# Kernel tuning notes

Hardware: AMD Instinct MI355X
Metric: run time of the kernel (lower is better)

## Reference

```python
import jax, jax.numpy as jnp
import numpy as np

N = 50000
E = 600000
D_IN = 128
D_HID = 128


def gcn_conv(x, src, dst, ew, W, b):
    """PyG-style GCNConv with self-loops and symmetric normalization.
    x: [N, Fin], src/dst: [E'], ew: [E'], W: [Fin, Fout], b: [Fout].
    """
    n = x.shape[0]
    # degree from incoming edge weights (self-loops already appended)
    deg = jax.ops.segment_sum(ew, dst, num_segments=n)
    dinv = jnp.where(deg > 0, jax.lax.rsqrt(deg), 0.0)
    norm = dinv[src] * ew * dinv[dst]  # [E']
    h = x @ W  # linear transform first (PyG order)
    msg = h[src] * norm[:, None]  # gather + scale, [E', Fout]
    out = jax.ops.segment_sum(msg, dst, num_segments=n)  # scatter-add
    return out + b


def setup_inputs() -> dict:
    key = jax.random.key(0)
    k1, k2, k3, k4, k5, k6, k7 = jax.random.split(key, 7)
    x = jax.random.normal(k1, (N, D_IN), dtype=jnp.float32)
    edge_index = jax.random.randint(k2, (2, E), 0, N, dtype=jnp.int64)
    edge_weight = jax.random.uniform(k3, (E,), dtype=jnp.float32)
    s1 = 1.0 / np.sqrt(D_IN)
    s2 = 1.0 / np.sqrt(D_HID)
    W1 = jax.random.uniform(k4, (D_IN, D_HID), dtype=jnp.float32, minval=-s1, maxval=s1)
    b1 = jax.random.uniform(k5, (D_HID,), dtype=jnp.float32, minval=-s1, maxval=s1)
    W2 = jax.random.uniform(k6, (D_HID, D_IN), dtype=jnp.float32, minval=-s2, maxval=s2)
    b2 = jax.random.uniform(k7, (D_IN,), dtype=jnp.float32, minval=-s2, maxval=s2)
    return {"x": x, "edge_index": edge_index, "edge_weight": edge_weight,
            "W1": W1, "b1": b1, "W2": W2, "b2": b2}


def reference(x, edge_index, edge_weight, W1, b1, W2, b2):
    n = x.shape[0]
    loops = jnp.arange(n, dtype=edge_index.dtype)
    src = jnp.concatenate([edge_index[0], loops])
    dst = jnp.concatenate([edge_index[1], loops])
    ew = jnp.concatenate([edge_weight, jnp.ones((n,), dtype=edge_weight.dtype)])
    h = gcn_conv(x, src, dst, ew, W1, b1)
    h = jax.nn.relu(h)
    h = gcn_conv(h, src, dst, ew, W2, b2)
    return jax.nn.sigmoid(h)
```

## Files before the change

kernel.cpp:

```cpp
#include <hip/hip_runtime.h>
#include <math.h>


typedef unsigned int uint32;
typedef unsigned long long u64;
typedef __attribute__((ext_vector_type(8))) short bf16x8;
typedef __attribute__((ext_vector_type(4))) float f32x4;
typedef __attribute__((ext_vector_type(2))) float f32x2;

__device__ __forceinline__ unsigned short f2bf(float f) {
    uint32 b = __float_as_uint(f);
    return (unsigned short)((b + 0x7FFFu + ((b >> 16) & 1u)) >> 16);
}

__device__ __forceinline__ float2 bf2_decode(uint32 u) {
    return make_float2(__uint_as_float(u << 16),
                       __uint_as_float(u & 0xFFFF0000u));
}

template <int AFP32, int OUTFP8>
__device__ __forceinline__ void gemm_body(const void* __restrict__ Ap,
                                          const unsigned short* __restrict__ WT,
                                          void* __restrict__ H,
                                          int n, int tb) {
    const int lane = threadIdx.x & 63;
    const int wv   = threadIdx.x >> 6;
    const int quad = lane >> 4;
    const int l16  = lane & 15;
    const int m0   = tb * 128 + wv * 32;
    f32x4 acc[2][8] = {};

    #pragma unroll
    for (int ks = 0; ks < 4; ++ks) {
        const int k0 = ks * 32 + quad * 8;
        bf16x8 a[2];
        #pragma unroll
        for (int rt = 0; rt < 2; ++rt) {
            int row = m0 + rt * 16 + l16;
            if (row >= n) row = n - 1;
            if (AFP32) {
                const float* Af = (const float*)Ap + (size_t)row * 128 + k0;
                float4 f0 = *(const float4*)(Af);
                float4 f1 = *(const float4*)(Af + 4);
                bf16x8 v;
                v[0] = (short)f2bf(f0.x); v[1] = (short)f2bf(f0.y);
                v[2] = (short)f2bf(f0.z); v[3] = (short)f2bf(f0.w);
                v[4] = (short)f2bf(f1.x); v[5] = (short)f2bf(f1.y);
                v[6] = (short)f2bf(f1.z); v[7] = (short)f2bf(f1.w);
                a[rt] = v;
            } else {
                const unsigned short* Ab = (const unsigned short*)Ap + (size_t)row * 128 + k0;
                a[rt] = *(const bf16x8*)Ab;
            }
        }
        #pragma unroll
        for (int ct = 0; ct < 8; ++ct) {
            bf16x8 b = *(const bf16x8*)(WT + (size_t)(ct * 16 + l16) * 128 + k0);
            acc[0][ct] = __builtin_amdgcn_mfma_f32_16x16x32_bf16(a[0], b, acc[0][ct], 0, 0, 0);
            acc[1][ct] = __builtin_amdgcn_mfma_f32_16x16x32_bf16(a[1], b, acc[1][ct], 0, 0, 0);
        }
    }

    #pragma unroll
    for (int rt = 0; rt < 2; ++rt) {
        #pragma unroll
        for (int r = 0; r < 4; ++r) {
            int row = m0 + rt * 16 + quad * 4 + r;
            if (row < n) {
                if (OUTFP8) {
                    unsigned char* o = (unsigned char*)H + (size_t)row * 128 + l16;
                    #pragma unroll
                    for (int cp = 0; cp < 4; ++cp) {
                        int pk = __builtin_amdgcn_cvt_pk_fp8_f32(
                            acc[rt][2 * cp][r], acc[rt][2 * cp + 1][r], 0, false);
                        o[(2 * cp) * 16]     = (unsigned char)(pk & 0xFF);
                        o[(2 * cp + 1) * 16] = (unsigned char)((pk >> 8) & 0xFF);
                    }
                } else {
                    unsigned short* o = (unsigned short*)H + (size_t)row * 128 + l16;
                    #pragma unroll
                    for (int ct = 0; ct < 8; ++ct)
                        o[ct * 16] = f2bf(acc[rt][ct][r]);
                }
            }
        }
    }
}

__global__ __launch_bounds__(256) void k_init(u64* __restrict__ packed, int n4,
                                              int* __restrict__ done,
                                              const float* __restrict__ W1,
                                              const float* __restrict__ W2,
                                              unsigned short* __restrict__ WT1,
                                              unsigned short* __restrict__ WT2) {
    int idx = blockIdx.x * 256 + threadIdx.x;
    if (idx < n4) ((uint4*)packed)[idx] = make_uint4(0u, 0u, 0u, 0u);
    if (idx == 0) *done = 0;
    if (blockIdx.x < 64) {
        int j = blockIdx.x * 256 + threadIdx.x;
        int k = j >> 7, nn = j & 127;
        WT1[nn * 128 + k] = f2bf(W1[k * 128 + nn]);
        WT2[nn * 128 + k] = f2bf(W2[k * 128 + nn]);
    }
}

__global__ __launch_bounds__(256) void k_gemm1_hist(const float* __restrict__ x,
                                                    const unsigned short* __restrict__ WT1,
                                                    unsigned char* __restrict__ h8,
                                                    const int* __restrict__ dst,
                                                    const float* __restrict__ ew,
                                                    u64* __restrict__ packed,
                                                    int* __restrict__ rank,
                                                    int E, int N, int gGemm) {
    const int b = blockIdx.x;
    if (b < gGemm) {
        gemm_body<1, 1>(x, WT1, h8, N, b);
        return;
    }
    int i = (b - gGemm) * 256 + threadIdx.x;
    if (i < E) {
        int d = dst[i];
        int r = (i >> 8) & 7;
        u64 add = (1ULL << 44) + (u64)(ew[i] * 4294967296.0f);
        u64 old = atomicAdd(&packed[(size_t)r * N + d], add);
        rank[i] = (int)(old >> 44);
    }
}

__global__ __launch_bounds__(256) void k_scan(const u64* __restrict__ packed,
                                              float* __restrict__ dinv,
                                              u64* __restrict__ bases,
                                              int* __restrict__ rowptr,
                                              int* __restrict__ csums,
                                              int* __restrict__ done, int nNodes) {
    __shared__ int s[256];
    __shared__ int lastFlag;
    const int t = threadIdx.x;
    const int base = blockIdx.x * 1024 + t * 4;
    const int n = nNodes + 1;
    int v[4];
    #pragma unroll
    for (int u = 0; u < 4; ++u) {
        int idx = base + u;
        int c = 0;
        if (idx < nNodes) {
            const u64 mask = (1ULL << 44) - 1;
            u64 ssum = 0;
            u64 bs = 0;
            uint32 cum = 0;
            #pragma unroll
            for (int r = 0; r < 8; ++r) {
                u64 pv = packed[(size_t)r * nNodes + idx];
                bs |= (u64)cum << (8 * r);
                cum += (uint32)(pv >> 44);
                ssum += (pv & mask);
            }
            c = (int)cum;
            float deg = 1.0f + (float)ssum * (1.0f / 4294967296.0f);
            dinv[idx] = rsqrtf(deg);
            bases[idx] = bs;
        }
        v[u] = c;
    }
    s[t] = v[0] + v[1] + v[2] + v[3];
    __syncthreads();
    #pragma unroll
    for (int off = 1; off < 256; off <<= 1) {
        int x = (t >= off) ? s[t - off] : 0;
        __syncthreads();
        s[t] += x;
        __syncthreads();
    }
    if (t == 255)
        __hip_atomic_store(&csums[blockIdx.x], s[255], __ATOMIC_RELEASE,
                           __HIP_MEMORY_SCOPE_AGENT);
    int e = (t == 0) ? 0 : s[t - 1];
    if (base + 0 < n) rowptr[base + 0] = e;
    if (base + 1 < n) rowptr[base + 1] = e + v[0];
    if (base + 2 < n) rowptr[base + 2] = e + v[0] + v[1];
    if (base + 3 < n) rowptr[base + 3] = e + v[0] + v[1] + v[2];

    __syncthreads();
    if (t == 0) {
        int prev = __hip_atomic_fetch_add(done, 1, __ATOMIC_ACQ_REL,
                                          __HIP_MEMORY_SCOPE_AGENT);
        lastFlag = (prev == (int)gridDim.x - 1);
    }
    __syncthreads();
    if (lastFlag && t < 64) {
        int g = (int)gridDim.x;
        int orig = (t < g) ? __hip_atomic_load(&csums[t], __ATOMIC_ACQUIRE,
                                               __HIP_MEMORY_SCOPE_AGENT)
                           : 0;
        int vv = orig;
        #pragma unroll
        for (int off = 1; off < 64; off <<= 1) {
            int y = __shfl_up(vv, off, 64);
            if (t >= off) vv += y;
        }
        if (t < g) csums[t] = vv - orig;
    }
}

__global__ __launch_bounds__(256) void k_fill(const int* __restrict__ src,
                                              const int* __restrict__ dst,
                                              const float* __restrict__ ew,
                                              const float* __restrict__ dinv,
                                              const int* __restrict__ rowptr,
                                              const int* __restrict__ csums,
                                              const u64* __restrict__ bases,
                                              const int* __restrict__ rank,
                                              float2* __restrict__ csr, int e) {
    int i = blockIdx.x * 256 + threadIdx.x;
    if (i < e) {
        int s = src[i], d = dst[i];
        int r = (i >> 8) & 7;
        float nrm = dinv[s] * ew[i] * dinv[d];
        int pos = rowptr[d] + csums[d >> 10]
                + (int)((bases[d] >> (8 * r)) & 0xFF) + rank[i];
        csr[pos] = make_float2(__int_as_float(s), nrm);
    }
}

__device__ __forceinline__ void fma8_bf(float* acc, uint4 u, float w) {
    float2 f;
    f = bf2_decode(u.x); acc[0] += f.x * w; acc[1] += f.y * w;
    f = bf2_decode(u.y); acc[2] += f.x * w; acc[3] += f.y * w;
    f = bf2_decode(u.z); acc[4] += f.x * w; acc[5] += f.y * w;
    f = bf2_decode(u.w); acc[6] += f.x * w; acc[7] += f.y * w;
}

__device__ __forceinline__ void fma8_f8(float* acc, uint2 u, float w) {
    f32x2 f;
    f = __builtin_amdgcn_cvt_pk_f32_fp8((int)u.x, false);
    acc[0] += f[0] * w; acc[1] += f[1] * w;
    f = __builtin_amdgcn_cvt_pk_f32_fp8((int)u.x, true);
    acc[2] += f[0] * w; acc[3] += f[1] * w;
    f = __builtin_amdgcn_cvt_pk_f32_fp8((int)u.y, false);
    acc[4] += f[0] * w; acc[5] += f[1] * w;
    f = __builtin_amdgcn_cvt_pk_f32_fp8((int)u.y, true);
    acc[6] += f[0] * w; acc[7] += f[1] * w;
}

__global__ __launch_bounds__(256) void k_ag2(const unsigned char* __restrict__ h8,
                                             const float2* __restrict__ csr,
                                             const int* __restrict__ rowptr,
                                             const int* __restrict__ csums,
                                             const float* __restrict__ dinv,
                                             const float4* __restrict__ bias4,
                                             const unsigned short* __restrict__ WT2,
                                             unsigned short* __restrict__ h2,
                                             int N) {
    __shared__ unsigned short sA[16][136];
    const int lane = threadIdx.x & 63;
    const int wv   = threadIdx.x >> 6;
    const int q    = lane >> 4;
    const int l    = lane & 15;
    const int nb   = blockIdx.x * 16;
    const uint2* H2 = (const uint2*)h8;

    for (int j = 0; j < 4; ++j) {
        const int node = nb + wv * 4 + j;
        float acc[8] = {};
        if (node < N) {
            const int start = rowptr[node] + csums[node >> 10];
            const int end   = rowptr[node + 1] + csums[(node + 1) >> 10];
            float di = dinv[node];
            float selfw = (q == 0) ? di * di : 0.0f;
            fma8_f8(acc, H2[(size_t)node * 16 + l], selfw);

            for (int k = start; k < end; k += 16) {
                float2 c[4];
                float w[4];
                #pragma unroll
                for (int jj = 0; jj < 4; ++jj) {
                    int ej = k + q + 4 * jj;
                    c[jj] = csr[ej < end ? ej : end - 1];
                    w[jj] = (ej < end) ? c[jj].y : 0.0f;
                }
                uint2 u[4];
                #pragma unroll
                for (int jj = 0; jj < 4; ++jj)
                    u[jj] = H2[(size_t)__float_as_int(c[jj].x) * 16 + l];
                #pragma unroll
                for (int jj = 0; jj < 4; ++jj) fma8_f8(acc, u[jj], w[jj]);
            }
            #pragma unroll
            for (int t = 0; t < 8; ++t) {
                acc[t] += __shfl_xor(acc[t], 16, 64);
                acc[t] += __shfl_xor(acc[t], 32, 64);
            }
        }
        if (q == 0) {
            uint4 o = make_uint4(0u, 0u, 0u, 0u);
            if (node < N) {
                float4 b0 = bias4[l * 2], b1v = bias4[l * 2 + 1];
                acc[0] += b0.x;  acc[1] += b0.y;  acc[2] += b0.z;  acc[3] += b0.w;
                acc[4] += b1v.x; acc[5] += b1v.y; acc[6] += b1v.z; acc[7] += b1v.w;
                #pragma unroll
                for (int t = 0; t < 8; ++t) acc[t] = fmaxf(acc[t], 0.0f);
                o.x = (uint32)f2bf(acc[0]) | ((uint32)f2bf(acc[1]) << 16);
                o.y = (uint32)f2bf(acc[2]) | ((uint32)f2bf(acc[3]) << 16);
                o.z = (uint32)f2bf(acc[4]) | ((uint32)f2bf(acc[5]) << 16);
                o.w = (uint32)f2bf(acc[6]) | ((uint32)f2bf(acc[7]) << 16);
            }
            *(uint4*)&sA[wv * 4 + j][l * 8] = o;
        }
    }

    __syncthreads();

    f32x4 a2[2] = {};
    #pragma unroll
    for (int ks = 0; ks < 4; ++ks) {
        const int k0 = ks * 32 + q * 8;
        bf16x8 a = *(const bf16x8*)&sA[l][k0];
        #pragma unroll
        for (int ct = 0; ct < 2; ++ct) {
            bf16x8 b = *(const bf16x8*)(WT2 + (size_t)(wv * 32 + ct * 16 + l) * 128 + k0);
            a2[ct] = __builtin_amdgcn_mfma_f32_16x16x32_bf16(a, b, a2[ct], 0, 0, 0);
        }
    }
    #pragma unroll
    for (int r = 0; r < 4; ++r) {
        int row = nb + q * 4 + r;
        if (row < N) {
            unsigned short* o = h2 + (size_t)row * 128 + wv * 32 + l;
            o[0]  = f2bf(a2[0][r]);
            o[16] = f2bf(a2[1][r]);
        }
    }
}

template <int INFP8, int ACT>
__global__ __launch_bounds__(256) void k_gather(const void* __restrict__ Hp,
                                                const float2* __restrict__ csr,
                                                const int* __restrict__ rowptr,
                                                const int* __restrict__ csums,
                                                const float* __restrict__ dinv,
                                                const float4* __restrict__ bias4,
                                                void* __restrict__ outp, int N) {
    int node = blockIdx.x * 4 + (threadIdx.x >> 6);
    if (node >= N) return;
    const int lane = threadIdx.x & 63;
    const int q = lane >> 4, l = lane & 15;
    const int start = rowptr[node] + csums[node >> 10];
    const int end   = rowptr[node + 1] + csums[(node + 1) >> 10];

    const uint2* H2 = (const uint2*)Hp;
    const uint4* H4 = (const uint4*)Hp;

    float di = dinv[node];
    float selfw = (q == 0) ? di * di : 0.0f;
    float acc[8] = {};
    if (INFP8) fma8_f8(acc, H2[(size_t)node * 16 + l], selfw);
    else       fma8_bf(acc, H4[(size_t)node * 16 + l], selfw);

    for (int k = start; k < end; k += 16) {
        float2 c[4];
        float w[4];
        #pragma unroll
        for (int j = 0; j < 4; ++j) {
            int ej = k + q + 4 * j;
            c[j] = csr[ej < end ? ej : end - 1];
            w[j] = (ej < end) ? c[j].y : 0.0f;
        }
        if (INFP8) {
            uint2 u[4];
            #pragma unroll
            for (int j = 0; j < 4; ++j)
                u[j] = H2[(size_t)__float_as_int(c[j].x) * 16 + l];
            #pragma unroll
            for (int j = 0; j < 4; ++j) fma8_f8(acc, u[j], w[j]);
        } else {
            uint4 u[4];
            #pragma unroll
            for (int j = 0; j < 4; ++j)
                u[j] = H4[(size_t)__float_as_int(c[j].x) * 16 + l];
            #pragma unroll
            for (int j = 0; j < 4; ++j) fma8_bf(acc, u[j], w[j]);
        }
    }

    #pragma unroll
    for (int j = 0; j < 8; ++j) {
        acc[j] += __shfl_xor(acc[j], 16, 64);
        acc[j] += __shfl_xor(acc[j], 32, 64);
    }

    if (q == 0) {
        float4 b0 = bias4[l * 2], b1 = bias4[l * 2 + 1];
        acc[0] += b0.x; acc[1] += b0.y; acc[2] += b0.z; acc[3] += b0.w;
        acc[4] += b1.x; acc[5] += b1.y; acc[6] += b1.z; acc[7] += b1.w;
        if (ACT == 0) {
            #pragma unroll
            for (int j = 0; j < 8; ++j) acc[j] = fmaxf(acc[j], 0.0f);
            uint4 o;
            o.x = (uint32)f2bf(acc[0]) | ((uint32)f2bf(acc[1]) << 16);
            o.y = (uint32)f2bf(acc[2]) | ((uint32)f2bf(acc[3]) << 16);
            o.z = (uint32)f2bf(acc[4]) | ((uint32)f2bf(acc[5]) << 16);
            o.w = (uint32)f2bf(acc[6]) | ((uint32)f2bf(acc[7]) << 16);
            ((uint4*)outp)[(size_t)node * 16 + l] = o;
        } else {
            #pragma unroll
            for (int j = 0; j < 8; ++j) acc[j] = 1.0f / (1.0f + expf(-acc[j]));
            float4* o4 = (float4*)outp + (size_t)node * 32 + l * 2;
            o4[0] = make_float4(acc[0], acc[1], acc[2], acc[3]);
            o4[1] = make_float4(acc[4], acc[5], acc[6], acc[7]);
        }
    }
}

extern "C" void kernel_launch(void* const* d_in, const int* in_sizes, int n_in,
                              void* d_out, int out_size, void* d_ws, size_t ws_size,
                              hipStream_t stream) {
    const float* x  = (const float*)d_in[0];
    const int*   ei = (const int*)d_in[1];
    const float* ew = (const float*)d_in[2];
    const float* W1 = (const float*)d_in[3];
    const float* b1 = (const float*)d_in[4];
    const float* W2 = (const float*)d_in[5];
    const float* b2 = (const float*)d_in[6];

    const int N = in_sizes[0] / 128;
    const int E = in_sizes[2];
    const int* src = ei;
    const int* dst = ei + E;
    float* out = (float*)d_out;

    auto align = [](size_t v) { return (v + 255) & ~(size_t)255; };
    char* p = (char*)d_ws;
    float*  dinv   = (float*)p;   p += align((size_t)N * 4);
    int*    rowptr = (int*)p;     p += align((size_t)(N + 1) * 4);
    int*    csums  = (int*)p;     p += align((size_t)1024 * 4);
    int*    done   = (int*)p;     p += align((size_t)256);
    u64*    bases  = (u64*)p;     p += align((size_t)N * 8);
    unsigned short* WT1 = (unsigned short*)p; p += align((size_t)128 * 128 * 2);
    unsigned short* WT2 = (unsigned short*)p; p += align((size_t)128 * 128 * 2);
    int*    rank   = (int*)p;     p += align((size_t)E * 4);
    float2* csr    = (float2*)p;  p += align((size_t)E * 8);
    unsigned char*  h8 = (unsigned char*)p;  p += align((size_t)N * 128);
    unsigned short* h2 = (unsigned short*)p;
    u64* packed = (u64*)h2;

    const int nbE = (E + 255) / 256;
    const int gScan = (N + 1 + 1023) / 1024;
    const int gGemm = (N + 127) / 128;
    const int gGath = (N + 3) / 4;
    const int gAg2  = (N + 15) / 16;
    const int n4 = N * 4;
    const int gInit = ((n4 + 255) / 256) < 64 ? 64 : ((n4 + 255) / 256);

    k_init<<<gInit, 256, 0, stream>>>(packed, n4, done, W1, W2, WT1, WT2);
    k_gemm1_hist<<<gGemm + nbE, 256, 0, stream>>>(x, WT1, h8, dst, ew, packed,
                                                  rank, E, N, gGemm);
    k_scan<<<gScan, 256, 0, stream>>>(packed, dinv, bases, rowptr, csums, done, N);
    k_fill<<<nbE, 256, 0, stream>>>(src, dst, ew, dinv, rowptr, csums, bases,
                                    rank, csr, E);

    k_ag2<<<gAg2, 256, 0, stream>>>(h8, csr, rowptr, csums, dinv,
                                    (const float4*)b1, WT2, h2, N);

    k_gather<0, 1><<<gGath, 256, 0, stream>>>(h2, csr, rowptr, csums,
                                              dinv, (const float4*)b2, out, N);
}
```

Measured before the change: 210.3 us.

## Reorder layer-2 as aggregate-then-transform with fp8 intermediate and fused sigmoid

Layer 1's aggregation now runs on its own and writes the ReLU output as fp8. Layer 2 then aggregates those fp8 features first and applies the W2 matmul with MFMA afterward, using the identity A(HW) = (AH)W. Bias and sigmoid are fused into the matmul epilogue, which removes the separate bf16 gather pass over h2. This halves the gather bytes in layer 2 (fp8 instead of bf16) and drops one intermediate write and read, but adds fp8 rounding on the hidden activations, which could hurt accuracy.

```diff
diff --git a/kernel.cpp b/kernel.cpp
--- a/kernel.cpp
+++ b/kernel.cpp
@@ -11,11 +11,6 @@
 __device__ __forceinline__ unsigned short f2bf(float f) {
     uint32 b = __float_as_uint(f);
     return (unsigned short)((b + 0x7FFFu + ((b >> 16) & 1u)) >> 16);
-}
-
-__device__ __forceinline__ float2 bf2_decode(uint32 u) {
-    return make_float2(__uint_as_float(u << 16),
-                       __uint_as_float(u & 0xFFFF0000u));
 }
 
 template <int AFP32, int OUTFP8>
@@ -222,14 +217,6 @@
     }
 }
 
-__device__ __forceinline__ void fma8_bf(float* acc, uint4 u, float w) {
-    float2 f;
-    f = bf2_decode(u.x); acc[0] += f.x * w; acc[1] += f.y * w;
-    f = bf2_decode(u.y); acc[2] += f.x * w; acc[3] += f.y * w;
-    f = bf2_decode(u.z); acc[4] += f.x * w; acc[5] += f.y * w;
-    f = bf2_decode(u.w); acc[6] += f.x * w; acc[7] += f.y * w;
-}
-
 __device__ __forceinline__ void fma8_f8(float* acc, uint2 u, float w) {
     f32x2 f;
     f = __builtin_amdgcn_cvt_pk_f32_fp8((int)u.x, false);
@@ -242,22 +229,80 @@
     acc[6] += f[0] * w; acc[7] += f[1] * w;
 }
 
-__global__ __launch_bounds__(256) void k_ag2(const unsigned char* __restrict__ h8,
+__global__ __launch_bounds__(256) void k_ag1(const unsigned char* __restrict__ h8,
                                              const float2* __restrict__ csr,
                                              const int* __restrict__ rowptr,
                                              const int* __restrict__ csums,
                                              const float* __restrict__ dinv,
                                              const float4* __restrict__ bias4,
-                                             const unsigned short* __restrict__ WT2,
-                                             unsigned short* __restrict__ h2,
-                                             int N) {
+                                             unsigned char* __restrict__ g8, int N) {
+    int node = blockIdx.x * 4 + (threadIdx.x >> 6);
+    if (node >= N) return;
+    const int lane = threadIdx.x & 63;
+    const int q = lane >> 4, l = lane & 15;
+    const int start = rowptr[node] + csums[node >> 10];
+    const int end   = rowptr[node + 1] + csums[(node + 1) >> 10];
+    const uint2* H2 = (const uint2*)h8;
+
+    float di = dinv[node];
+    float selfw = (q == 0) ? di * di : 0.0f;
+    float acc[8] = {};
+    fma8_f8(acc, H2[(size_t)node * 16 + l], selfw);
+
+    for (int k = start; k < end; k += 16) {
+        float2 c[4];
+        float w[4];
+        #pragma unroll
+        for (int j = 0; j < 4; ++j) {
+            int ej = k + q + 4 * j;
+            c[j] = csr[ej < end ? ej : end - 1];
+            w[j] = (ej < end) ? c[j].y : 0.0f;
+        }
+        uint2 u[4];
+        #pragma unroll
+        for (int j = 0; j < 4; ++j)
+            u[j] = H2[(size_t)__float_as_int(c[j].x) * 16 + l];
+        #pragma unroll
+        for (int j = 0; j < 4; ++j) fma8_f8(acc, u[j], w[j]);
+    }
+
+    #pragma unroll
+    for (int j = 0; j < 8; ++j) {
+        acc[j] += __shfl_xor(acc[j], 16, 64);
+        acc[j] += __shfl_xor(acc[j], 32, 64);
+    }
+
+    if (q == 0) {
+        float4 b0 = bias4[l * 2], b1v = bias4[l * 2 + 1];
+        acc[0] += b0.x;  acc[1] += b0.y;  acc[2] += b0.z;  acc[3] += b0.w;
+        acc[4] += b1v.x; acc[5] += b1v.y; acc[6] += b1v.z; acc[7] += b1v.w;
+        #pragma unroll
+        for (int j = 0; j < 8; ++j) acc[j] = fmaxf(acc[j], 0.0f);
+        uint2 o;
+        int w0 = __builtin_amdgcn_cvt_pk_fp8_f32(acc[0], acc[1], 0, false);
+        w0     = __builtin_amdgcn_cvt_pk_fp8_f32(acc[2], acc[3], w0, true);
+        int w1 = __builtin_amdgcn_cvt_pk_fp8_f32(acc[4], acc[5], 0, false);
+        w1     = __builtin_amdgcn_cvt_pk_fp8_f32(acc[6], acc[7], w1, true);
+        o.x = (uint32)w0; o.y = (uint32)w1;
+        ((uint2*)g8)[(size_t)node * 16 + l] = o;
+    }
+}
+
+__global__ __launch_bounds__(256) void k_ag2s(const unsigned char* __restrict__ g8,
+                                              const float2* __restrict__ csr,
+                                              const int* __restrict__ rowptr,
+                                              const int* __restrict__ csums,
+                                              const float* __restrict__ dinv,
+                                              const float* __restrict__ b2,
+                                              const unsigned short* __restrict__ WT2,
+                                              float* __restrict__ out, int N) {
     __shared__ unsigned short sA[16][136];
     const int lane = threadIdx.x & 63;
     const int wv   = threadIdx.x >> 6;
     const int q    = lane >> 4;
     const int l    = lane & 15;
     const int nb   = blockIdx.x * 16;
-    const uint2* H2 = (const uint2*)h8;
+    const uint2* G2 = (const uint2*)g8;
 
     for (int j = 0; j < 4; ++j) {
         const int node = nb + wv * 4 + j;
@@ -267,7 +312,7 @@
             const int end   = rowptr[node + 1] + csums[(node + 1) >> 10];
             float di = dinv[node];
             float selfw = (q == 0) ? di * di : 0.0f;
-            fma8_f8(acc, H2[(size_t)node * 16 + l], selfw);
+            fma8_f8(acc, G2[(size_t)node * 16 + l], selfw);
 
             for (int k = start; k < end; k += 16) {
                 float2 c[4];
@@ -281,7 +326,7 @@
                 uint2 u[4];
                 #pragma unroll
                 for (int jj = 0; jj < 4; ++jj)
-                    u[jj] = H2[(size_t)__float_as_int(c[jj].x) * 16 + l];
+                    u[jj] = G2[(size_t)__float_as_int(c[jj].x) * 16 + l];
                 #pragma unroll
                 for (int jj = 0; jj < 4; ++jj) fma8_f8(acc, u[jj], w[jj]);
             }
@@ -294,11 +339,6 @@
         if (q == 0) {
             uint4 o = make_uint4(0u, 0u, 0u, 0u);
             if (node < N) {
-                float4 b0 = bias4[l * 2], b1v = bias4[l * 2 + 1];
-                acc[0] += b0.x;  acc[1] += b0.y;  acc[2] += b0.z;  acc[3] += b0.w;
-                acc[4] += b1v.x; acc[5] += b1v.y; acc[6] += b1v.z; acc[7] += b1v.w;
-                #pragma unroll
-                for (int t = 0; t < 8; ++t) acc[t] = fmaxf(acc[t], 0.0f);
                 o.x = (uint32)f2bf(acc[0]) | ((uint32)f2bf(acc[1]) << 16);
                 o.y = (uint32)f2bf(acc[2]) | ((uint32)f2bf(acc[3]) << 16);
                 o.z = (uint32)f2bf(acc[4]) | ((uint32)f2bf(acc[5]) << 16);
@@ -322,91 +362,16 @@
         }
     }
     #pragma unroll
-    for (int r = 0; r < 4; ++r) {
-        int row = nb + q * 4 + r;
-        if (row < N) {
-            unsigned short* o = h2 + (size_t)row * 128 + wv * 32 + l;
-            o[0]  = f2bf(a2[0][r]);
-            o[16] = f2bf(a2[1][r]);
-        }
-    }
-}
-
-template <int INFP8, int ACT>
-__global__ __launch_bounds__(256) void k_gather(const void* __restrict__ Hp,
-                                                const float2* __restrict__ csr,
-                                                const int* __restrict__ rowptr,
-                                                const int* __restrict__ csums,
-                                                const float* __restrict__ dinv,
-                                                const float4* __restrict__ bias4,
-                                                void* __restrict__ outp, int N) {
-    int node = blockIdx.x * 4 + (threadIdx.x >> 6);
-    if (node >= N) return;
-    const int lane = threadIdx.x & 63;
-    const int q = lane >> 4, l = lane & 15;
-    const int start = rowptr[node] + csums[node >> 10];
-    const int end   = rowptr[node + 1] + csums[(node + 1) >> 10];
-
-    const uint2* H2 = (const uint2*)Hp;
-    const uint4* H4 = (const uint4*)Hp;
-
-    float di = dinv[node];
-    float selfw = (q == 0) ? di * di : 0.0f;
-    float acc[8] = {};
-    if (INFP8) fma8_f8(acc, H2[(size_t)node * 16 + l], selfw);
-    else       fma8_bf(acc, H4[(size_t)node * 16 + l], selfw);
-
-    for (int k = start; k < end; k += 16) {
-        float2 c[4];
-        float w[4];
-        #pragma unroll
-        for (int j = 0; j < 4; ++j) {
-            int ej = k + q + 4 * j;
-            c[j] = csr[ej < end ? ej : end - 1];
-            w[j] = (ej < end) ? c[j].y : 0.0f;
-        }
-        if (INFP8) {
-            uint2 u[4];
-            #pragma unroll
-            for (int j = 0; j < 4; ++j)
-                u[j] = H2[(size_t)__float_as_int(c[j].x) * 16 + l];
-            #pragma unroll
-            for (int j = 0; j < 4; ++j) fma8_f8(acc, u[j], w[j]);
-        } else {
-            uint4 u[4];
-            #pragma unroll
-            for (int j = 0; j < 4; ++j)
-                u[j] = H4[(size_t)__float_as_int(c[j].x) * 16 + l];
-            #pragma unroll
-            for (int j = 0; j < 4; ++j) fma8_bf(acc, u[j], w[j]);
-        }
-    }
-
-    #pragma unroll
-    for (int j = 0; j < 8; ++j) {
-        acc[j] += __shfl_xor(acc[j], 16, 64);
-        acc[j] += __shfl_xor(acc[j], 32, 64);
-    }
-
-    if (q == 0) {
-        float4 b0 = bias4[l * 2], b1 = bias4[l * 2 + 1];
-        acc[0] += b0.x; acc[1] += b0.y; acc[2] += b0.z; acc[3] += b0.w;
-        acc[4] += b1.x; acc[5] += b1.y; acc[6] += b1.z; acc[7] += b1.w;
-        if (ACT == 0) {
-            #pragma unroll
-            for (int j = 0; j < 8; ++j) acc[j] = fmaxf(acc[j], 0.0f);
-            uint4 o;
-            o.x = (uint32)f2bf(acc[0]) | ((uint32)f2bf(acc[1]) << 16);
-            o.y = (uint32)f2bf(acc[2]) | ((uint32)f2bf(acc[3]) << 16);
-            o.z = (uint32)f2bf(acc[4]) | ((uint32)f2bf(acc[5]) << 16);
-            o.w = (uint32)f2bf(acc[6]) | ((uint32)f2bf(acc[7]) << 16);
-            ((uint4*)outp)[(size_t)node * 16 + l] = o;
-        } else {
-            #pragma unroll
-            for (int j = 0; j < 8; ++j) acc[j] = 1.0f / (1.0f + expf(-acc[j]));
-            float4* o4 = (float4*)outp + (size_t)node * 32 + l * 2;
-            o4[0] = make_float4(acc[0], acc[1], acc[2], acc[3]);
-            o4[1] = make_float4(acc[4], acc[5], acc[6], acc[7]);
+    for (int ct = 0; ct < 2; ++ct) {
+        const int col = wv * 32 + ct * 16 + l;
+        const float bb = b2[col];
+        #pragma unroll
+        for (int r = 0; r < 4; ++r) {
+            int row = nb + q * 4 + r;
+            if (row < N) {
+                float v = a2[ct][r] + bb;
+                out[(size_t)row * 128 + col] = 1.0f / (1.0f + expf(-v));
+            }
         }
     }
 }
@@ -440,13 +405,13 @@
     int*    rank   = (int*)p;     p += align((size_t)E * 4);
     float2* csr    = (float2*)p;  p += align((size_t)E * 8);
     unsigned char*  h8 = (unsigned char*)p;  p += align((size_t)N * 128);
-    unsigned short* h2 = (unsigned short*)p;
-    u64* packed = (u64*)h2;
+    unsigned char*  g8 = (unsigned char*)p;
+    u64* packed = (u64*)g8;
 
     const int nbE = (E + 255) / 256;
     const int gScan = (N + 1 + 1023) / 1024;
     const int gGemm = (N + 127) / 128;
-    const int gGath = (N + 3) / 4;
+    const int gAg1  = (N + 3) / 4;
     const int gAg2  = (N + 15) / 16;
     const int n4 = N * 4;
     const int gInit = ((n4 + 255) / 256) < 64 ? 64 : ((n4 + 255) / 256);
@@ -458,9 +423,9 @@
     k_fill<<<nbE, 256, 0, stream>>>(src, dst, ew, dinv, rowptr, csums, bases,
                                     rank, csr, E);
 
-    k_ag2<<<gAg2, 256, 0, stream>>>(h8, csr, rowptr, csums, dinv,
-                                    (const float4*)b1, WT2, h2, N);
-
-    k_gather<0, 1><<<gGath, 256, 0, stream>>>(h2, csr, rowptr, csums,
-                                              dinv, (const float4*)b2, out, N);
-}
+    k_ag1<<<gAg1, 256, 0, stream>>>(h8, csr, rowptr, csums, dinv,
+                                    (const float4*)b1, g8, N);
+
+    k_ag2s<<<gAg2, 256, 0, stream>>>(g8, csr, rowptr, csums, dinv, b2,
+                                     WT2, out, N);
+}
```

Result: faster. 201.5 us (-4.2%).
